# Kernel tuning notes

Measured on AMD Instinct MI355X. Metric: run time of the kernel, lower is better.

The kernel has to match this reference:

```python
import jax, jax.numpy as jnp
import numpy as np

B, S, D = 8, 1024, 256
H, DH = 8, 32  # num_heads, head_dim; H*DH == D


def setup_inputs() -> dict:
    key = jax.random.key(0)
    ks = jax.random.split(key, 10)
    s = 0.02
    return {
        "q": jax.random.normal(ks[0], (B, S, D), jnp.float32),
        "k": jax.random.normal(ks[1], (B, S, D), jnp.float32),
        "v": jax.random.normal(ks[2], (B, S, D), jnp.float32),
        "mask": jnp.zeros((B, 1, 1, S), jnp.float32),  # additive mask
        "bias": jax.random.normal(ks[3], (1, H, S, S), jnp.float32),  # pair bias
        "Wq": jax.random.normal(ks[4], (H * DH, D), jnp.float32) * s,
        "Wk": jax.random.normal(ks[5], (H * DH, D), jnp.float32) * s,
        "Wv": jax.random.normal(ks[6], (H * DH, D), jnp.float32) * s,
        "Wg": jnp.zeros((H * DH, D), jnp.float32),   # gating init: zeros weight
        "bg": jnp.ones((H * DH,), jnp.float32),      # gating init: ones bias
        "Wo": jax.random.normal(ks[7], (D, H * DH), jnp.float32) * s,
    }


def reference(q, k, v, mask, bias, Wq, Wk, Wv, Wg, bg, Wo):
    norm = DH ** -0.5
    g = jnp.einsum('bsd,ed->bse', q, Wg) + bg            # [B,S,H*DH]
    qh = (jnp.einsum('bsd,ed->bse', q, Wq) * norm).reshape(B, S, H, DH)
    kh = jnp.einsum('bsd,ed->bse', k, Wk).reshape(B, S, H, DH)
    vh = jnp.einsum('bsd,ed->bse', v, Wv).reshape(B, S, H, DH)
    # scores [B,H,Q,K] with additive mask and pair bias (unicore softmax_dropout)
    attn = jnp.einsum('bqhd,bkhd->bhqk', qh, kh) + mask + bias
    attn = jax.nn.softmax(attn, axis=-1)
    o = jnp.einsum('bhqk,bkhd->bqhd', attn, vh).reshape(B, S, H * DH)
    o = jax.nn.sigmoid(g) * o                            # gating
    return jnp.einsum('bse,de->bsd', o, Wo)              # output proj, NO bias in fwd
```

## Files before the change

### kernel.cpp

```cpp
#include <hip/hip_runtime.h>


typedef __attribute__((ext_vector_type(4))) float f32x4;
typedef __attribute__((ext_vector_type(16))) float f32x16;
typedef __attribute__((ext_vector_type(8))) unsigned short u16x8;
typedef __attribute__((ext_vector_type(4))) unsigned short u16x4;
typedef __attribute__((ext_vector_type(8))) __bf16 bf16x8;
typedef __attribute__((ext_vector_type(4))) __bf16 bf16x4;

#define BB 8
#define SS 1024
#define DD 256
#define HH 8
#define DHD 32
#define L2E 1.4426950408889634f

__device__ __forceinline__ float b2f(unsigned short s) {
  unsigned u = ((unsigned)s) << 16;
  return __builtin_bit_cast(float, u);
}
__device__ __forceinline__ f32x4 mfma16(u16x8 a, u16x8 b, f32x4 c) {
  return __builtin_amdgcn_mfma_f32_16x16x32_bf16(
      __builtin_bit_cast(bf16x8, a), __builtin_bit_cast(bf16x8, b), c, 0, 0, 0);
}
__device__ __forceinline__ f32x16 mfma32(u16x8 a, u16x8 b, f32x16 c) {
  return __builtin_amdgcn_mfma_f32_32x32x16_bf16(
      __builtin_bit_cast(bf16x8, a), __builtin_bit_cast(bf16x8, b), c, 0, 0, 0);
}

__device__ __forceinline__ void gload_lds16(const unsigned short* gsrc,
                                            unsigned short* ldst) {
#if __has_builtin(__builtin_amdgcn_global_load_lds)
  __builtin_amdgcn_global_load_lds(
      (const __attribute__((address_space(1))) unsigned int*)gsrc,
      (__attribute__((address_space(3))) unsigned int*)ldst, 16, 0, 0);
#else
  *(u16x8*)ldst = *(const u16x8*)gsrc;
#endif
}

__global__ __launch_bounds__(256) void proj_kernel(
    const float* __restrict__ q, const float* __restrict__ k,
    const float* __restrict__ v,
    const float* __restrict__ Wq, const float* __restrict__ Wg,
    const float* __restrict__ Wk, const float* __restrict__ Wv,
    const float* __restrict__ bg,
    unsigned short* __restrict__ qh, unsigned short* __restrict__ kh,
    unsigned short* __restrict__ vhT, unsigned short* __restrict__ sig) {
  const int slot = blockIdx.z;
  const float* A = (slot <= 1) ? q : (slot == 2 ? k : v);
  const float* W = (slot == 0) ? Wq : (slot == 1 ? Wg : (slot == 2 ? Wk : Wv));
  const int row0 = blockIdx.x * 64, col0 = blockIdx.y * 64;
  const int tid = threadIdx.x;
  const int w = tid >> 6, lane = tid & 63, g = lane >> 4, c = lane & 15;
  const int sr = tid >> 2, sc = tid & 3;

  __shared__ alignas(16) unsigned short As[64 * 32];
  __shared__ alignas(16) unsigned short Ws[64 * 32];

  const f32x4 zero = {0.f, 0.f, 0.f, 0.f};
  f32x4 acc[4] = {zero, zero, zero, zero};

  for (int kk = 0; kk < 8; ++kk) {
    __syncthreads();
    {
      const float* ap = A + (size_t)(row0 + sr) * DD + kk * 32 + sc * 8;
      f32x4 f0 = *(const f32x4*)ap;
      f32x4 f1 = *(const f32x4*)(ap + 4);
      bf16x8 a8;
#pragma unroll
      for (int j = 0; j < 4; ++j) { a8[j] = (__bf16)f0[j]; a8[j + 4] = (__bf16)f1[j]; }
      ((u16x8*)As)[sr * 4 + (sc ^ ((sr >> 1) & 3))] = __builtin_bit_cast(u16x8, a8);

      const float* wp = W + (size_t)(col0 + sr) * DD + kk * 32 + sc * 8;
      f32x4 w0 = *(const f32x4*)wp;
      f32x4 w1 = *(const f32x4*)(wp + 4);
      bf16x8 w8;
#pragma unroll
      for (int j = 0; j < 4; ++j) { w8[j] = (__bf16)w0[j]; w8[j + 4] = (__bf16)w1[j]; }
      ((u16x8*)Ws)[sr * 4 + (sc ^ ((sr >> 1) & 3))] = __builtin_bit_cast(u16x8, w8);
    }
    __syncthreads();
    const int arow = 16 * w + c;
    u16x8 af = ((u16x8*)As)[arow * 4 + (g ^ ((arow >> 1) & 3))];
#pragma unroll
    for (int n = 0; n < 4; ++n) {
      const int brow = 16 * n + c;
      u16x8 wf = ((u16x8*)Ws)[brow * 4 + (g ^ ((brow >> 1) & 3))];
      acc[n] = mfma16(af, wf, acc[n]);
    }
  }

  if (slot == 3) {
    const int row_base = row0 + 16 * w + 4 * g;
    const int bb = row_base >> 10;
    const int s0 = row_base & 1023;
#pragma unroll
    for (int n = 0; n < 4; ++n) {
      const int col = col0 + 16 * n + c;
      bf16x4 pv;
#pragma unroll
      for (int r = 0; r < 4; ++r) pv[r] = (__bf16)acc[n][r];
      *(u16x4*)(vhT + (size_t)(bb * 256 + col) * SS + s0) =
          __builtin_bit_cast(u16x4, pv);
    }
  } else {
#pragma unroll
    for (int n = 0; n < 4; ++n) {
#pragma unroll
      for (int r = 0; r < 4; ++r) {
        const int row = row0 + 16 * w + 4 * g + r;
        const int col = col0 + 16 * n + c;
        const size_t idx = (size_t)row * DD + col;
        const float val = acc[n][r];
        if (slot == 0)
          qh[idx] = __builtin_bit_cast(unsigned short,
                        (__bf16)(val * 0.17677669529663687f));
        else if (slot == 1)
          sig[idx] = __builtin_bit_cast(unsigned short,
                         (__bf16)(1.0f / (1.0f + __expf(-(val + bg[col])))));
        else
          kh[idx] = __builtin_bit_cast(unsigned short, (__bf16)val);
      }
    }
  }
}

__global__ __launch_bounds__(128, 2) void attn_kernel(
    const unsigned short* __restrict__ qh, const unsigned short* __restrict__ kh,
    const unsigned short* __restrict__ vhT, const unsigned short* __restrict__ sig,
    const float* __restrict__ mask, const float* __restrict__ bias,
    unsigned short* __restrict__ og) {
  const int bid = blockIdx.x;
  const int widx = (bid & 7) * 128 + (bid >> 3);
  const int h = widx >> 7, b = (widx >> 4) & 7, qt = widx & 15;
  const int tid = threadIdx.x;
  const int w = tid >> 6, lane = tid & 63;
  const int qc = lane & 31, hi = lane >> 5;

  __shared__ alignas(16) unsigned short KsB[2][64 * 32];
  __shared__ alignas(16) unsigned short VtB[2][32 * 64];

  const int qrow = qt * 64 + w * 32 + qc;
  const unsigned short* qp = qh + (size_t)(b * SS + qrow) * DD + h * DHD;
  const u16x8 qf0 = *(const u16x8*)(qp + 8 * hi);
  const u16x8 qf1 = *(const u16x8*)(qp + 16 + 8 * hi);

  f32x16 acc = {};
  float m_r = -1e30f, l_r = 0.f;

  const float* maskb = mask + b * SS;
  const float* biasq = bias + ((size_t)h * SS + qrow) * SS;

  auto stage = [&](int buf, int kv0) {
    unsigned short* Kb = KsB[buf];
    unsigned short* Vb = VtB[buf];
#pragma unroll
    for (int i = 0; i < 2; ++i) {
      const int s = i * 128 + tid;
      const int kr = s >> 2, pc = s & 3;
      gload_lds16(
          kh + (size_t)(b * SS + kv0 + kr) * DD + h * DHD + (pc ^ (kr & 3)) * 8,
          Kb + s * 8);
      const int vr = s >> 3, pj = s & 7;
      const int lu = (2 * pj) ^ ((vr & 7) << 1);
      gload_lds16(
          vhT + (size_t)((b * HH + h) * DHD + vr) * SS + kv0 + lu * 4,
          Vb + s * 8);
    }
  };

  stage(0, 0);
  __syncthreads();

#pragma unroll 1
  for (int kt = 0; kt < 16; ++kt) {
    const int cur = kt & 1, kv0 = kt * 64;

    f32x4 bm[2][4];
#pragma unroll
    for (int t = 0; t < 2; ++t)
#pragma unroll
      for (int rq = 0; rq < 4; ++rq) {
        const int off = kv0 + 32 * t + 8 * rq + 4 * hi;
        const f32x4 bi = *(const f32x4*)(biasq + off);
        const f32x4 mk = *(const f32x4*)(maskb + off);
        bm[t][rq] = bi + mk;
      }

    if (kt < 15) stage(cur ^ 1, kv0 + 64);

    const unsigned short* Kb = KsB[cur];
    const unsigned short* Vb = VtB[cur];

    f32x16 sv[2];
#pragma unroll
    for (int t = 0; t < 2; ++t) {
      const int kr = 32 * t + qc;
      const u16x8 ka = ((const u16x8*)Kb)[kr * 4 + (hi ^ (kr & 3))];
      const u16x8 kb2 = ((const u16x8*)Kb)[kr * 4 + ((2 + hi) ^ (kr & 3))];
      f32x16 z = {};
      z = mfma32(ka, qf0, z);
      sv[t] = mfma32(kb2, qf1, z);
    }

#pragma unroll
    for (int t = 0; t < 2; ++t)
#pragma unroll
      for (int rq = 0; rq < 4; ++rq)
#pragma unroll
        for (int j = 0; j < 4; ++j) sv[t][4 * rq + j] += bm[t][rq][j];

    float pm = sv[0][0];
#pragma unroll
    for (int j = 1; j < 16; ++j) pm = fmaxf(pm, sv[0][j]);
#pragma unroll
    for (int j = 0; j < 16; ++j) pm = fmaxf(pm, sv[1][j]);
    if (!__all(pm - m_r <= 8.0f)) {
      const float mx = fmaxf(pm, __shfl_xor(pm, 32));
      const float mnew = fmaxf(m_r, mx);
      const float sc = exp2f((m_r - mnew) * L2E);
      l_r *= sc;
      acc = acc * sc;
      m_r = mnew;
    }

    const float nm = -m_r * L2E;
    float ps = 0.f;
#pragma unroll
    for (int t = 0; t < 2; ++t)
#pragma unroll
      for (int j = 0; j < 16; ++j) {
        const float p = exp2f(__builtin_fmaf(sv[t][j], L2E, nm));
        sv[t][j] = p;
        ps += p;
      }
    l_r += ps;

#pragma unroll
    for (int t = 0; t < 2; ++t) {
      bf16x8 p0, p1;
#pragma unroll
      for (int j = 0; j < 8; ++j) {
        p0[j] = (__bf16)sv[t][j];
        p1[j] = (__bf16)sv[t][8 + j];
      }
#pragma unroll
      for (int ks = 0; ks < 2; ++ks) {
        const int u1 = 8 * t + 4 * ks + hi;
        const int sw = (qc & 7) << 1;
        const u16x4 va = *(const u16x4*)(Vb + qc * 64 + (u1 ^ sw) * 4);
        const u16x4 vb2 = *(const u16x4*)(Vb + qc * 64 + ((u1 | 2) ^ sw) * 4);
        const u16x8 vf = {va[0], va[1], va[2], va[3],
                          vb2[0], vb2[1], vb2[2], vb2[3]};
        acc = mfma32(vf, __builtin_bit_cast(u16x8, ks == 0 ? p0 : p1), acc);
      }
    }

    __syncthreads();
  }

  const float lp = l_r + __shfl_xor(l_r, 32);
  const float inv = 1.0f / lp;
#pragma unroll
  for (int rq = 0; rq < 4; ++rq) {
    const int dh0 = 8 * rq + 4 * hi;
    const size_t idx = (size_t)(b * SS + qrow) * DD + h * DHD + dh0;
    const u16x4 sg = *(const u16x4*)(sig + idx);
    bf16x4 ov;
#pragma unroll
    for (int j = 0; j < 4; ++j)
      ov[j] = (__bf16)(acc[4 * rq + j] * inv * b2f(sg[j]));
    *(u16x4*)(og + idx) = __builtin_bit_cast(u16x4, ov);
  }
}

__global__ __launch_bounds__(256) void outproj_kernel(
    const unsigned short* __restrict__ og, const float* __restrict__ Wo,
    float* __restrict__ out) {
  const int row0 = blockIdx.x * 64, col0 = blockIdx.y * 64;
  const int tid = threadIdx.x;
  const int w = tid >> 6, lane = tid & 63, g = lane >> 4, c = lane & 15;
  const int sr = tid >> 2, sc = tid & 3;

  __shared__ alignas(16) unsigned short As[64 * 32];
  __shared__ alignas(16) unsigned short Ws[64 * 32];

  const f32x4 zero = {0.f, 0.f, 0.f, 0.f};
  f32x4 acc[4] = {zero, zero, zero, zero};

  for (int kk = 0; kk < 8; ++kk) {
    __syncthreads();
    {
      const unsigned short* ap = og + (size_t)(row0 + sr) * DD + kk * 32 + sc * 8;
      ((u16x8*)As)[sr * 4 + (sc ^ ((sr >> 1) & 3))] = *(const u16x8*)ap;

      const float* wp = Wo + (size_t)(col0 + sr) * DD + kk * 32 + sc * 8;
      f32x4 w0 = *(const f32x4*)wp;
      f32x4 w1 = *(const f32x4*)(wp + 4);
      bf16x8 w8;
#pragma unroll
      for (int j = 0; j < 4; ++j) { w8[j] = (__bf16)w0[j]; w8[j + 4] = (__bf16)w1[j]; }
      ((u16x8*)Ws)[sr * 4 + (sc ^ ((sr >> 1) & 3))] = __builtin_bit_cast(u16x8, w8);
    }
    __syncthreads();
    const int arow = 16 * w + c;
    u16x8 af = ((u16x8*)As)[arow * 4 + (g ^ ((arow >> 1) & 3))];
#pragma unroll
    for (int n = 0; n < 4; ++n) {
      const int brow = 16 * n + c;
      u16x8 wf = ((u16x8*)Ws)[brow * 4 + (g ^ ((brow >> 1) & 3))];
      acc[n] = mfma16(af, wf, acc[n]);
    }
  }

#pragma unroll
  for (int n = 0; n < 4; ++n) {
#pragma unroll
    for (int r = 0; r < 4; ++r) {
      const int row = row0 + 16 * w + 4 * g + r;
      const int col = col0 + 16 * n + c;
      out[(size_t)row * DD + col] = acc[n][r];
    }
  }
}

extern "C" void kernel_launch(void* const* d_in, const int* in_sizes, int n_in,
                              void* d_out, int out_size, void* d_ws,
                              size_t ws_size, hipStream_t stream) {
  const float* q    = (const float*)d_in[0];
  const float* k    = (const float*)d_in[1];
  const float* v    = (const float*)d_in[2];
  const float* mask = (const float*)d_in[3];
  const float* bias = (const float*)d_in[4];
  const float* Wq   = (const float*)d_in[5];
  const float* Wk   = (const float*)d_in[6];
  const float* Wv   = (const float*)d_in[7];
  const float* Wg   = (const float*)d_in[8];
  const float* bg   = (const float*)d_in[9];
  const float* Wo   = (const float*)d_in[10];
  float* out = (float*)d_out;

  char* ws = (char*)d_ws;
  unsigned short* qh  = (unsigned short*)(ws);
  unsigned short* kh  = (unsigned short*)(ws + (4u << 20));
  unsigned short* vhT = (unsigned short*)(ws + (8u << 20));
  unsigned short* sig = (unsigned short*)(ws + (12u << 20));
  unsigned short* og  = (unsigned short*)(ws + (16u << 20));

  hipLaunchKernelGGL(proj_kernel, dim3(128, 4, 4), dim3(256), 0, stream,
                     q, k, v, Wq, Wg, Wk, Wv, bg, qh, kh, vhT, sig);
  hipLaunchKernelGGL(attn_kernel, dim3(1024), dim3(128), 0, stream,
                     qh, kh, vhT, sig, mask, bias, og);
  hipLaunchKernelGGL(outproj_kernel, dim3(128, 4), dim3(256), 0, stream,
                     og, Wo, out);
}
```

Baseline: 87.70 us.

## Share pair-bias tile across batches in LDS; read K/V directly from global

Restructures the attention kernel so each 512-thread block handles one head and one 32-query tile across all 8 batch elements, one wave per batch. The pair bias, which does not depend on batch, is staged once per block into a double-buffered LDS tile and reused by all eight waves, cutting bias global traffic by a factor of eight. K and V are no longer staged through LDS; each wave loads its fragments directly from global memory. The risks are uncoalesced, unswizzled direct K/V loads, fewer blocks (256) and a transposed LDS bias store that may hit bank conflicts.

New measurement: 99.84 us. 1.14x slower.

```diff
diff --git a/kernel.cpp b/kernel.cpp
--- a/kernel.cpp
+++ b/kernel.cpp
@@ -26,17 +26,6 @@
 __device__ __forceinline__ f32x16 mfma32(u16x8 a, u16x8 b, f32x16 c) {
   return __builtin_amdgcn_mfma_f32_32x32x16_bf16(
       __builtin_bit_cast(bf16x8, a), __builtin_bit_cast(bf16x8, b), c, 0, 0, 0);
-}
-
-__device__ __forceinline__ void gload_lds16(const unsigned short* gsrc,
-                                            unsigned short* ldst) {
-#if __has_builtin(__builtin_amdgcn_global_load_lds)
-  __builtin_amdgcn_global_load_lds(
-      (const __attribute__((address_space(1))) unsigned int*)gsrc,
-      (__attribute__((address_space(3))) unsigned int*)ldst, 16, 0, 0);
-#else
-  *(u16x8*)ldst = *(const u16x8*)gsrc;
-#endif
 }
 
 __global__ __launch_bounds__(256) void proj_kernel(
@@ -126,22 +115,20 @@
   }
 }
 
-__global__ __launch_bounds__(128, 2) void attn_kernel(
+__global__ __launch_bounds__(512) void attn_kernel(
     const unsigned short* __restrict__ qh, const unsigned short* __restrict__ kh,
     const unsigned short* __restrict__ vhT, const unsigned short* __restrict__ sig,
     const float* __restrict__ mask, const float* __restrict__ bias,
     unsigned short* __restrict__ og) {
   const int bid = blockIdx.x;
-  const int widx = (bid & 7) * 128 + (bid >> 3);
-  const int h = widx >> 7, b = (widx >> 4) & 7, qt = widx & 15;
+  const int h = bid & 7, qt = bid >> 3;
   const int tid = threadIdx.x;
-  const int w = tid >> 6, lane = tid & 63;
+  const int b = tid >> 6, lane = tid & 63;
   const int qc = lane & 31, hi = lane >> 5;
 
-  __shared__ alignas(16) unsigned short KsB[2][64 * 32];
-  __shared__ alignas(16) unsigned short VtB[2][32 * 64];
-
-  const int qrow = qt * 64 + w * 32 + qc;
+  __shared__ float biasS[2][64][36];
+
+  const int qrow = qt * 32 + qc;
   const unsigned short* qp = qh + (size_t)(b * SS + qrow) * DD + h * DHD;
   const u16x8 qf0 = *(const u16x8*)(qp + 8 * hi);
   const u16x8 qf1 = *(const u16x8*)(qp + 16 + 8 * hi);
@@ -150,55 +137,37 @@
   float m_r = -1e30f, l_r = 0.f;
 
   const float* maskb = mask + b * SS;
-  const float* biasq = bias + ((size_t)h * SS + qrow) * SS;
-
-  auto stage = [&](int buf, int kv0) {
-    unsigned short* Kb = KsB[buf];
-    unsigned short* Vb = VtB[buf];
-#pragma unroll
-    for (int i = 0; i < 2; ++i) {
-      const int s = i * 128 + tid;
-      const int kr = s >> 2, pc = s & 3;
-      gload_lds16(
-          kh + (size_t)(b * SS + kv0 + kr) * DD + h * DHD + (pc ^ (kr & 3)) * 8,
-          Kb + s * 8);
-      const int vr = s >> 3, pj = s & 7;
-      const int lu = (2 * pj) ^ ((vr & 7) << 1);
-      gload_lds16(
-          vhT + (size_t)((b * HH + h) * DHD + vr) * SS + kv0 + lu * 4,
-          Vb + s * 8);
-    }
-  };
-
-  stage(0, 0);
+  const unsigned short* kbase = kh + (size_t)(b * SS) * DD + h * DHD;
+  const unsigned short* vbase = vhT + (size_t)((b * HH + h) * DHD + qc) * SS;
+
+  const int srow = tid >> 4, schunk = tid & 15;
+  const float* bsrc =
+      bias + ((size_t)(h * SS + qt * 32 + srow)) * SS + schunk * 4;
+
+  {
+    const f32x4 v4 = *(const f32x4*)(bsrc);
+#pragma unroll
+    for (int i = 0; i < 4; ++i) biasS[0][schunk * 4 + i][srow] = v4[i];
+  }
   __syncthreads();
 
 #pragma unroll 1
   for (int kt = 0; kt < 16; ++kt) {
     const int cur = kt & 1, kv0 = kt * 64;
 
-    f32x4 bm[2][4];
-#pragma unroll
-    for (int t = 0; t < 2; ++t)
-#pragma unroll
-      for (int rq = 0; rq < 4; ++rq) {
-        const int off = kv0 + 32 * t + 8 * rq + 4 * hi;
-        const f32x4 bi = *(const f32x4*)(biasq + off);
-        const f32x4 mk = *(const f32x4*)(maskb + off);
-        bm[t][rq] = bi + mk;
-      }
-
-    if (kt < 15) stage(cur ^ 1, kv0 + 64);
-
-    const unsigned short* Kb = KsB[cur];
-    const unsigned short* Vb = VtB[cur];
+    if (kt < 15) {
+      const f32x4 v4 = *(const f32x4*)(bsrc + kv0 + 64);
+#pragma unroll
+      for (int i = 0; i < 4; ++i)
+        biasS[cur ^ 1][schunk * 4 + i][srow] = v4[i];
+    }
 
     f32x16 sv[2];
 #pragma unroll
     for (int t = 0; t < 2; ++t) {
-      const int kr = 32 * t + qc;
-      const u16x8 ka = ((const u16x8*)Kb)[kr * 4 + (hi ^ (kr & 3))];
-      const u16x8 kb2 = ((const u16x8*)Kb)[kr * 4 + ((2 + hi) ^ (kr & 3))];
+      const unsigned short* kp = kbase + (size_t)(kv0 + 32 * t + qc) * DD;
+      const u16x8 ka = *(const u16x8*)(kp + 8 * hi);
+      const u16x8 kb2 = *(const u16x8*)(kp + 16 + 8 * hi);
       f32x16 z = {};
       z = mfma32(ka, qf0, z);
       sv[t] = mfma32(kb2, qf1, z);
@@ -207,9 +176,13 @@
 #pragma unroll
     for (int t = 0; t < 2; ++t)
 #pragma unroll
-      for (int rq = 0; rq < 4; ++rq)
-#pragma unroll
-        for (int j = 0; j < 4; ++j) sv[t][4 * rq + j] += bm[t][rq][j];
+      for (int rq = 0; rq < 4; ++rq) {
+        const int kvl = 32 * t + 8 * rq + 4 * hi;
+        const f32x4 mk = *(const f32x4*)(maskb + kv0 + kvl);
+#pragma unroll
+        for (int j = 0; j < 4; ++j)
+          sv[t][4 * rq + j] += biasS[cur][kvl + j][qc] + mk[j];
+      }
 
     float pm = sv[0][0];
 #pragma unroll
@@ -248,9 +221,8 @@
 #pragma unroll
       for (int ks = 0; ks < 2; ++ks) {
         const int u1 = 8 * t + 4 * ks + hi;
-        const int sw = (qc & 7) << 1;
-        const u16x4 va = *(const u16x4*)(Vb + qc * 64 + (u1 ^ sw) * 4);
-        const u16x4 vb2 = *(const u16x4*)(Vb + qc * 64 + ((u1 | 2) ^ sw) * 4);
+        const u16x4 va = *(const u16x4*)(vbase + kv0 + u1 * 4);
+        const u16x4 vb2 = *(const u16x4*)(vbase + kv0 + (u1 | 2) * 4);
         const u16x8 vf = {va[0], va[1], va[2], va[3],
                           vb2[0], vb2[1], vb2[2], vb2[3]};
         acc = mfma32(vf, __builtin_bit_cast(u16x8, ks == 0 ? p0 : p1), acc);
@@ -350,7 +322,7 @@
 
   hipLaunchKernelGGL(proj_kernel, dim3(128, 4, 4), dim3(256), 0, stream,
                      q, k, v, Wq, Wg, Wk, Wv, bg, qh, kh, vhT, sig);
-  hipLaunchKernelGGL(attn_kernel, dim3(1024), dim3(128), 0, stream,
+  hipLaunchKernelGGL(attn_kernel, dim3(256), dim3(512), 0, stream,
                      qh, kh, vhT, sig, mask, bias, og);
   hipLaunchKernelGGL(outproj_kernel, dim3(128, 4), dim3(256), 0, stream,
                      og, Wo, out);
```
